# Optimization experiments

Measured on AMD Instinct MI355X. Metric: run time of the kernel, lower is better.

The kernel has to match this reference:

```python
import jax, jax.numpy as jnp
import numpy as np

EPS = 1e-05  # norm_epsilon

def setup_inputs() -> dict:
    key = jax.random.key(0)
    ks = jax.random.split(key, 6)
    B, T, D, E, N, C = 16, 512, 256, 16, 8192, 1
    xs = jax.random.normal(ks[0], (B, T, D), jnp.float32)
    pad_mask = jnp.ones((B, T), dtype=bool)
    masked_masks = jax.random.randint(ks[1], (B, T), 0, 2) > 0
    ln_gamma = jnp.ones((D,), jnp.float32)
    ln_beta = jnp.zeros((D,), jnp.float32)
    # xavier_normal init for the (frozen) random projection
    projection = jax.random.normal(ks[2], (D, E), jnp.float32) * (2.0 / (D + E)) ** 0.5
    embeddings = jax.random.normal(ks[3], (C, E, N), jnp.float32)
    top_n_out = jax.random.normal(ks[4], (C, D, N), jnp.float32) * 0.02
    mask_emb = jax.random.normal(ks[5], (D,), jnp.float32) * 0.1
    return {"xs": xs, "pad_mask": pad_mask, "masked_masks": masked_masks,
            "ln_gamma": ln_gamma, "ln_beta": ln_beta, "projection": projection,
            "embeddings": embeddings, "top_n_out": top_n_out, "mask_emb": mask_emb}

def reference(xs, pad_mask, masked_masks, ln_gamma, ln_beta, projection, embeddings, top_n_out, mask_emb):
    B, T, D = xs.shape
    C = embeddings.shape[0]
    # ---- target path: layer norm -> random projection -> nearest codebook idx ----
    mu = jnp.mean(xs, -1, keepdims=True)
    var = jnp.mean((xs - mu) ** 2, -1, keepdims=True)
    h = (xs - mu) / jnp.sqrt(var + EPS) * ln_gamma + ln_beta
    proj = jnp.einsum('btd,de->bte', h, projection).reshape(B * T, -1)  # [BT,E]
    # pairwise squared distances: [C, BT, N]
    dist = (jnp.sum(proj ** 2, axis=1)[None, :, None]
            + jnp.sum(embeddings ** 2, axis=1)[:, None, :]
            - 2.0 * jnp.einsum('te,cen->ctn', proj, embeddings))
    target = jnp.argmin(dist, axis=-1).T.reshape(B, T, C)  # [B,T,C] int
    # ---- masked input -> encoder (identity stand-in) -> per-codebook logits ----
    masked_xs = jnp.where(masked_masks[..., None], mask_emb, xs)
    logits = jnp.einsum('btd,cdn->btcn', masked_xs, top_n_out)  # [B,T,C,N]
    logp = jax.nn.log_softmax(logits, axis=-1)
    ce = -jnp.take_along_axis(logp, target[..., None], axis=-1)[..., 0]  # [B,T,C]
    m = (pad_mask & masked_masks).astype(logits.dtype)  # [B,T]
    loss = jnp.sum(ce * m[..., None]) / (jnp.sum(m) * C)
    return loss
```

## Files before the change

### kernel.cpp

```cpp
#include <hip/hip_runtime.h>
#include <hip/hip_bf16.h>
#include <math.h>

#define BT   8192
#define DD   256
#define EE   16
#define NN   8192

typedef __attribute__((ext_vector_type(8))) short short8;
typedef __attribute__((ext_vector_type(4))) float f32x4;

__device__ __forceinline__ unsigned short f2bf(float x) {
  union { float f; unsigned int u; } c; c.f = x;
  unsigned int r = (c.u + 0x7FFFu + ((c.u >> 16) & 1u)) >> 16;
  return (unsigned short)r;
}
__device__ __forceinline__ unsigned int ordf(float d) {
  union { float f; unsigned int u; } c; c.f = d;
  return ((int)c.u < 0) ? ~c.u : (c.u | 0x80000000u);
}
__device__ __forceinline__ unsigned long long shflxor64(unsigned long long v, int m) {
  unsigned int lo = (unsigned int)v, hi = (unsigned int)(v >> 32);
  lo = __shfl_xor((int)lo, m);
  hi = __shfl_xor((int)hi, m);
  return ((unsigned long long)hi << 32) | lo;
}
__device__ __forceinline__ void gload_lds16(const void* g, void* l) {
  __builtin_amdgcn_global_load_lds((const __attribute__((address_space(1))) void*)g,
                                   (__attribute__((address_space(3))) void*)l, 16, 0, 0);
}

#define XT_LD 65
__global__ __launch_bounds__(256) void k_pre(const float* __restrict__ xs,
                                             const int* __restrict__ mm,
                                             const float* __restrict__ memb,
                                             const float* __restrict__ gamma,
                                             const float* __restrict__ beta,
                                             const float* __restrict__ P,
                                             const float* __restrict__ W,
                                             const float* __restrict__ emb,
                                             unsigned short* __restrict__ xmb,
                                             unsigned short* __restrict__ projb,
                                             unsigned short* __restrict__ Wt,
                                             unsigned short* __restrict__ embT,
                                             float* __restrict__ sqe,
                                             unsigned long long* __restrict__ keys,
                                             float* __restrict__ sumexp) {
  __shared__ __align__(16) float xt[32 * XT_LD * 4];
  __shared__ float stats[32][2];
  __shared__ __align__(16) float Pl[DD * EE];
  __shared__ __align__(16) float gl[DD], bl[DD];
  int bid = blockIdx.x;
  int tid = threadIdx.x;

  if (bid < 512) {
    int n0 = (bid & 127) * 64;
    int d0 = (bid >> 7) * 64;
    #pragma unroll
    for (int pass = 0; pass < 16; pass++) {
      int idx = pass * 256 + tid;
      int dd = idx >> 6, ln = idx & 63;
      xt[ln * 65 + dd] = W[(size_t)(d0 + dd) * NN + n0 + ln];
    }
    __syncthreads();
    #pragma unroll
    for (int pass = 0; pass < 2; pass++) {
      int g = pass * 256 + tid;
      int row = g >> 3, c8 = g & 7;
      short8 v;
      #pragma unroll
      for (int i = 0; i < 8; i++) v[i] = (short)f2bf(xt[row * 65 + c8 * 8 + i]);
      *(short8*)(Wt + (size_t)(n0 + row) * DD + d0 + c8 * 8) = v;
    }
    return;
  }
  if (bid < 544) {
    int n = (bid - 512) * 256 + tid;
    float e[EE];
    float sq = 0.f;
    #pragma unroll
    for (int k = 0; k < EE; k++) { e[k] = emb[k * NN + n]; sq += e[k] * e[k]; }
    short8 lo, hi;
    #pragma unroll
    for (int k = 0; k < 8; k++) { lo[k] = (short)f2bf(e[k]); hi[k] = (short)f2bf(e[k + 8]); }
    *(short8*)(embT + (size_t)n * EE)     = lo;
    *(short8*)(embT + (size_t)n * EE + 8) = hi;
    sqe[n] = 0.5f * sq;
    keys[n] = ~0ULL;
    return;
  }
  int pb = bid - 544;
  int t0 = pb * 32;
  int w = tid >> 6;
  int col4 = tid & 63;
  float4 mb4 = ((const float4*)memb)[col4];

  #pragma unroll
  for (int i = tid; i < DD * EE / 4; i += 256)
    ((float4*)Pl)[i] = ((const float4*)P)[i];
  if (tid < DD / 4) {
    ((float4*)gl)[tid] = ((const float4*)gamma)[tid];
    ((float4*)bl)[tid] = ((const float4*)beta)[tid];
  }

  #pragma unroll
  for (int j = 0; j < 8; j++) {
    int k = tid + j * 256;
    int row = w + j * 4;
    float4 xv = ((const float4*)xs)[(size_t)pb * 2048 + k];
    int m = mm[t0 + row];
    float4 v = m ? mb4 : xv;
    ushort2 o01 = { f2bf(v.x), f2bf(v.y) };
    ushort2 o23 = { f2bf(v.z), f2bf(v.w) };
    ((ushort2*)(xmb + (size_t)(t0 + row) * DD + col4 * 4))[0] = o01;
    ((ushort2*)(xmb + (size_t)(t0 + row) * DD + col4 * 4))[1] = o23;
    *(float4*)&xt[(row * XT_LD + col4) * 4] = xv;
  }
  __syncthreads();
  {
    int t = tid >> 3, g = tid & 7;
    float s = 0.f, s2 = 0.f;
    #pragma unroll
    for (int i = 0; i < 8; i++) {
      float4 v = *(const float4*)&xt[(t * XT_LD + g * 8 + i) * 4];
      s  += v.x + v.y + v.z + v.w;
      s2 += v.x * v.x + v.y * v.y + v.z * v.z + v.w * v.w;
    }
    #pragma unroll
    for (int m = 1; m <= 4; m <<= 1) { s += __shfl_xor(s, m); s2 += __shfl_xor(s2, m); }
    if (g == 0) {
      float mu = s * (1.0f / DD);
      float var = s2 * (1.0f / DD) - mu * mu;
      stats[t][0] = mu;
      stats[t][1] = rsqrtf(var + 1e-5f);
    }
  }
  if (tid < 32) sumexp[t0 + tid] = 0.f;
  __syncthreads();
  {
    int t = tid >> 3, e0 = (tid & 7) * 2;
    float mu = stats[t][0], rstd = stats[t][1];
    float a0 = 0.f, a1 = 0.f;
    for (int d = 0; d < DD; d += 4) {
      float4 xv = *(const float4*)&xt[(t * XT_LD + (d >> 2)) * 4];
      float xd[4] = { xv.x, xv.y, xv.z, xv.w };
      #pragma unroll
      for (int dd = 0; dd < 4; dd++) {
        float h = (xd[dd] - mu) * rstd * gl[d + dd] + bl[d + dd];
        a0 += h * Pl[(d + dd) * EE + e0];
        a1 += h * Pl[(d + dd) * EE + e0 + 1];
      }
    }
    ushort2 o = { f2bf(a0), f2bf(a1) };
    *(ushort2*)(projb + (size_t)(t0 + t) * EE + e0) = o;
  }
}

#define NS4 8
#define ASEG (NN / NS4)
__global__ __launch_bounds__(256) void k_argmin(const unsigned short* __restrict__ projb,
                                                const unsigned short* __restrict__ embT,
                                                const float* __restrict__ sqe,
                                                unsigned long long* __restrict__ keys) {
  int tid = threadIdx.x;
  int w = tid >> 6, lane = tid & 63;
  int q = lane >> 4, c = lane & 15;
  int tw = blockIdx.x * 64 + w * 16;
  int nseg = blockIdx.y * ASEG;

  short8 a = {0, 0, 0, 0, 0, 0, 0, 0};
  if (q < 2) a = *(const short8*)(projb + (size_t)(tw + c) * EE + q * 8);

  unsigned int bo[4], bi[4];
  #pragma unroll
  for (int r = 0; r < 4; r++) { bo[r] = 0xFFFFFFFFu; bi[r] = 0u; }

  #pragma unroll 2
  for (int it = 0; it < ASEG / 16; it++) {
    int n = nseg + it * 16 + c;
    short8 b = {0, 0, 0, 0, 0, 0, 0, 0};
    if (q < 2) b = *(const short8*)(embT + (size_t)n * EE + q * 8);
    float sqh = sqe[n];
    f32x4 acc = (f32x4){0.f, 0.f, 0.f, 0.f};
    acc = __builtin_amdgcn_mfma_f32_16x16x32_bf16(a, b, acc, 0, 0, 0);
    #pragma unroll
    for (int r = 0; r < 4; r++) {
      float dist = sqh - acc[r];
      unsigned int u = ordf(dist);
      if (u < bo[r]) { bo[r] = u; bi[r] = (unsigned int)n; }
    }
  }
  unsigned long long bk[4];
  #pragma unroll
  for (int r = 0; r < 4; r++)
    bk[r] = ((unsigned long long)bo[r] << 32) | bi[r];
  #pragma unroll
  for (int r = 0; r < 4; r++) {
    #pragma unroll
    for (int m = 1; m <= 8; m <<= 1) {
      unsigned long long o = shflxor64(bk[r], m);
      bk[r] = o < bk[r] ? o : bk[r];
    }
  }
  if (c == 0) {
    #pragma unroll
    for (int r = 0; r < 4; r++)
      atomicMin(&keys[tw + q * 4 + r], bk[r]);
  }
}

__global__ __launch_bounds__(512, 4) void k_ce5(const unsigned short* __restrict__ xmb,
                                                const unsigned short* __restrict__ Wt,
                                                const unsigned long long* __restrict__ keys,
                                                float* __restrict__ sumexp,
                                                float* __restrict__ ltar) {
  __shared__ __align__(16) unsigned short ldsA[3][128 * 32];
  __shared__ __align__(16) unsigned short ldsB[3][128 * 32];
  int tid = threadIdx.x;
  int lane = tid & 63;
  int w = tid >> 6;
  int q = lane >> 4, c = lane & 15;
  int wm = w >> 1, wn = w & 1;
  int t0 = blockIdx.x * 128;
  int n0 = blockIdx.y * 128;
  int sw = q ^ ((c >> 1) & 3);

  f32x4 acc[2][4];
  #pragma unroll
  for (int mi = 0; mi < 2; mi++)
    #pragma unroll
    for (int ni = 0; ni < 4; ni++) acc[mi][ni] = (f32x4){0.f, 0.f, 0.f, 0.f};

  #define STAGE(buf, itv) do {                                                  \
    int kk_ = (itv) * 32;                                                       \
    int g = tid;                                                                \
    int row = g >> 2;                                                           \
    int qg = (g & 3) ^ ((g >> 3) & 3);                                          \
    gload_lds16(xmb + (size_t)(t0 + row) * DD + kk_ + qg * 8,                   \
                ldsA[buf] + g * 8);                                             \
    gload_lds16(Wt + (size_t)(n0 + row) * DD + kk_ + qg * 8,                    \
                ldsB[buf] + g * 8);                                             \
  } while (0)

  STAGE(0, 0);
  STAGE(1, 1);
  asm volatile("s_waitcnt vmcnt(2)" ::: "memory");
  __builtin_amdgcn_s_barrier();

  #pragma unroll
  for (int it = 0; it < 8; it++) {
    const int cur = it % 3;
    const int nxt = (it + 2) % 3;
    if (it + 2 < 8) {
      if (nxt == 0)      STAGE(0, it + 2);
      else if (nxt == 1) STAGE(1, it + 2);
      else               STAGE(2, it + 2);
    }

    short8 a[2], b[4];
    #pragma unroll
    for (int mi = 0; mi < 2; mi++)
      a[mi] = *(const short8*)(ldsA[cur] + (wm * 32 + mi * 16 + c) * 32 + sw * 8);
    #pragma unroll
    for (int ni = 0; ni < 4; ni++)
      b[ni] = *(const short8*)(ldsB[cur] + (wn * 64 + ni * 16 + c) * 32 + sw * 8);
    #pragma unroll
    for (int mi = 0; mi < 2; mi++)
      #pragma unroll
      for (int ni = 0; ni < 4; ni++)
        acc[mi][ni] = __builtin_amdgcn_mfma_f32_16x16x32_bf16(a[mi], b[ni], acc[mi][ni], 0, 0, 0);

    if (it < 6) {
      asm volatile("s_waitcnt vmcnt(2)" ::: "memory");
      __builtin_amdgcn_s_barrier();
    } else if (it == 6) {
      asm volatile("s_waitcnt vmcnt(0)" ::: "memory");
      __builtin_amdgcn_s_barrier();
    }
  }
  #undef STAGE

  int tg[2][4];
  #pragma unroll
  for (int mi = 0; mi < 2; mi++)
    #pragma unroll
    for (int r = 0; r < 4; r++)
      tg[mi][r] = (int)(unsigned int)(keys[t0 + wm * 32 + mi * 16 + q * 4 + r] & 0xFFFFFFFFULL);

  float rs[2][4];
  #pragma unroll
  for (int mi = 0; mi < 2; mi++)
    #pragma unroll
    for (int r = 0; r < 4; r++) rs[mi][r] = 0.f;

  #pragma unroll
  for (int mi = 0; mi < 2; mi++)
    #pragma unroll
    for (int ni = 0; ni < 4; ni++) {
      int col = n0 + wn * 64 + ni * 16 + c;
      #pragma unroll
      for (int r = 0; r < 4; r++) {
        float v = acc[mi][ni][r];
        if (col == tg[mi][r])
          ltar[t0 + wm * 32 + mi * 16 + q * 4 + r] = v;
        rs[mi][r] += __expf(v);
      }
    }

  #pragma unroll
  for (int mi = 0; mi < 2; mi++)
    #pragma unroll
    for (int r = 0; r < 4; r++) {
      float s = rs[mi][r];
      s += __shfl_xor(s, 1);
      s += __shfl_xor(s, 2);
      s += __shfl_xor(s, 4);
      s += __shfl_xor(s, 8);
      if (c == 0)
        atomicAdd(&sumexp[t0 + wm * 32 + mi * 16 + q * 4 + r], s);
    }
}

__global__ __launch_bounds__(1024) void k_final(const float* __restrict__ sumexp,
                                                const float* __restrict__ ltar,
                                                const int* __restrict__ padm,
                                                const int* __restrict__ mm,
                                                float* __restrict__ out) {
  int tid = threadIdx.x;
  float sum = 0.f, cnt = 0.f;
  for (int t = tid; t < BT; t += 1024) {
    float ce = __logf(sumexp[t]) - ltar[t];
    if (padm[t] && mm[t]) { sum += ce; cnt += 1.f; }
  }
  #pragma unroll
  for (int off = 32; off; off >>= 1) { sum += __shfl_down(sum, off); cnt += __shfl_down(cnt, off); }
  __shared__ float rs[16], rc[16];
  int wid = tid >> 6, lane = tid & 63;
  if (lane == 0) { rs[wid] = sum; rc[wid] = cnt; }
  __syncthreads();
  if (tid == 0) {
    float S = 0.f, Cn = 0.f;
    for (int i = 0; i < 16; i++) { S += rs[i]; Cn += rc[i]; }
    out[0] = S / Cn;
  }
}

extern "C" void kernel_launch(void* const* d_in, const int* in_sizes, int n_in,
                              void* d_out, int out_size, void* d_ws, size_t ws_size,
                              hipStream_t stream) {
  const float* xs    = (const float*)d_in[0];
  const int*   padm  = (const int*)d_in[1];
  const int*   mm    = (const int*)d_in[2];
  const float* gamma = (const float*)d_in[3];
  const float* beta  = (const float*)d_in[4];
  const float* P     = (const float*)d_in[5];
  const float* emb   = (const float*)d_in[6];
  const float* W     = (const float*)d_in[7];
  const float* memb  = (const float*)d_in[8];
  float* out = (float*)d_out;

  char* ws = (char*)d_ws;
  size_t off = 0;
  unsigned short* xmb   = (unsigned short*)(ws + off); off += (size_t)BT * DD * 2;
  unsigned short* Wtb   = (unsigned short*)(ws + off); off += (size_t)NN * DD * 2;
  unsigned short* embT  = (unsigned short*)(ws + off); off += (size_t)NN * EE * 2;
  unsigned short* projb = (unsigned short*)(ws + off); off += (size_t)BT * EE * 2;
  float* sqe            = (float*)(ws + off);          off += (size_t)NN * 4;
  unsigned long long* keys = (unsigned long long*)(ws + off); off += (size_t)BT * 8;
  float* sumexp         = (float*)(ws + off);          off += (size_t)BT * 4;
  float* ltar           = (float*)(ws + off);          off += (size_t)BT * 4;

  k_pre   <<<800, 256, 0, stream>>>(xs, mm, memb, gamma, beta, P, W, emb,
                                    xmb, projb, Wtb, embT, sqe, keys, sumexp);
  k_argmin<<<dim3(BT / 64, NS4), 256, 0, stream>>>(projb, embT, sqe, keys);
  k_ce5   <<<dim3(64, 64), 512, 0, stream>>>(xmb, Wtb, keys, sumexp, ltar);
  k_final <<<1, 1024, 0, stream>>>(sumexp, ltar, padm, mm, out);
}
```

Baseline: 170.5 us.

## Load full K tile into LDS at once instead of triple-buffered pipeline

Replaces the 3-stage K-pipelined staging of A and B tiles with one bulk load of the whole 128x256 A and B tiles into LDS (128KB total), followed by a single barrier and a barrier-free MFMA loop. It uses a new XOR swizzle over 16-byte chunks and lowers launch bounds to 2 blocks per CU. This removes the per-iteration barriers and waitcnts but gives up overlap of loads with compute inside a block and reduces occupancy because of the much larger LDS footprint.

```diff
diff --git a/kernel.cpp b/kernel.cpp
--- a/kernel.cpp
+++ b/kernel.cpp
@@ -209,13 +209,13 @@
   }
 }
 
-__global__ __launch_bounds__(512, 4) void k_ce5(const unsigned short* __restrict__ xmb,
+__global__ __launch_bounds__(512, 2) void k_ce5(const unsigned short* __restrict__ xmb,
                                                 const unsigned short* __restrict__ Wt,
                                                 const unsigned long long* __restrict__ keys,
                                                 float* __restrict__ sumexp,
                                                 float* __restrict__ ltar) {
-  __shared__ __align__(16) unsigned short ldsA[3][128 * 32];
-  __shared__ __align__(16) unsigned short ldsB[3][128 * 32];
+  __shared__ __align__(16) unsigned short ldsA[128 * 256];
+  __shared__ __align__(16) unsigned short ldsB[128 * 256];
   int tid = threadIdx.x;
   int lane = tid & 63;
   int w = tid >> 6;
@@ -223,7 +223,6 @@
   int wm = w >> 1, wn = w & 1;
   int t0 = blockIdx.x * 128;
   int n0 = blockIdx.y * 128;
-  int sw = q ^ ((c >> 1) & 3);
 
   f32x4 acc[2][4];
   #pragma unroll
@@ -231,54 +230,38 @@
     #pragma unroll
     for (int ni = 0; ni < 4; ni++) acc[mi][ni] = (f32x4){0.f, 0.f, 0.f, 0.f};
 
-  #define STAGE(buf, itv) do {                                                  \
-    int kk_ = (itv) * 32;                                                       \
-    int g = tid;                                                                \
-    int row = g >> 2;                                                           \
-    int qg = (g & 3) ^ ((g >> 3) & 3);                                          \
-    gload_lds16(xmb + (size_t)(t0 + row) * DD + kk_ + qg * 8,                   \
-                ldsA[buf] + g * 8);                                             \
-    gload_lds16(Wt + (size_t)(n0 + row) * DD + kk_ + qg * 8,                    \
-                ldsB[buf] + g * 8);                                             \
-  } while (0)
-
-  STAGE(0, 0);
-  STAGE(1, 1);
-  asm volatile("s_waitcnt vmcnt(2)" ::: "memory");
+  #pragma unroll
+  for (int j = 0; j < 8; j++) {
+    int g = j * 512 + tid;
+    int row = g >> 5, s = g & 31;
+    int ck = (s & 24) | ((s & 7) ^ (row & 7));
+    gload_lds16(xmb + (size_t)(t0 + row) * DD + ck * 8, ldsA + g * 8);
+    gload_lds16(Wt + (size_t)(n0 + row) * DD + ck * 8, ldsB + g * 8);
+  }
+  asm volatile("s_waitcnt vmcnt(0)" ::: "memory");
   __builtin_amdgcn_s_barrier();
 
   #pragma unroll
-  for (int it = 0; it < 8; it++) {
-    const int cur = it % 3;
-    const int nxt = (it + 2) % 3;
-    if (it + 2 < 8) {
-      if (nxt == 0)      STAGE(0, it + 2);
-      else if (nxt == 1) STAGE(1, it + 2);
-      else               STAGE(2, it + 2);
-    }
-
-    short8 a[2], b[4];
-    #pragma unroll
-    for (int mi = 0; mi < 2; mi++)
-      a[mi] = *(const short8*)(ldsA[cur] + (wm * 32 + mi * 16 + c) * 32 + sw * 8);
-    #pragma unroll
-    for (int ni = 0; ni < 4; ni++)
-      b[ni] = *(const short8*)(ldsB[cur] + (wn * 64 + ni * 16 + c) * 32 + sw * 8);
-    #pragma unroll
-    for (int mi = 0; mi < 2; mi++)
+  for (int kk = 0; kk < 8; kk++) {
+    short8 a[2];
+    #pragma unroll
+    for (int mi = 0; mi < 2; mi++) {
+      int row = wm * 32 + mi * 16 + c;
+      int ck = kk * 4 + q;
+      int s = (ck & 24) | ((ck & 7) ^ (row & 7));
+      a[mi] = *(const short8*)(ldsA + row * 256 + s * 8);
+    }
+    #pragma unroll
+    for (int ni = 0; ni < 4; ni++) {
+      int col = wn * 64 + ni * 16 + c;
+      int ck = kk * 4 + q;
+      int s = (ck & 24) | ((ck & 7) ^ (col & 7));
+      short8 b = *(const short8*)(ldsB + col * 256 + s * 8);
       #pragma unroll
-      for (int ni = 0; ni < 4; ni++)
-        acc[mi][ni] = __builtin_amdgcn_mfma_f32_16x16x32_bf16(a[mi], b[ni], acc[mi][ni], 0, 0, 0);
-
-    if (it < 6) {
-      asm volatile("s_waitcnt vmcnt(2)" ::: "memory");
-      __builtin_amdgcn_s_barrier();
-    } else if (it == 6) {
-      asm volatile("s_waitcnt vmcnt(0)" ::: "memory");
-      __builtin_amdgcn_s_barrier();
-    }
-  }
-  #undef STAGE
+      for (int mi = 0; mi < 2; mi++)
+        acc[mi][ni] = __builtin_amdgcn_mfma_f32_16x16x32_bf16(a[mi], b, acc[mi][ni], 0, 0, 0);
+    }
+  }
 
   int tg[2][4];
   #pragma unroll
```

Result: slower. 207.9 us (+21.9%).
